# Optimization experiments

Hardware: AMD Instinct MI355X
Metric: run time of the kernel (lower is better)

The kernel has to match this reference:

```python
import jax, jax.numpy as jnp
import numpy as np
from jax import lax

L1_DECAY = 1e-06


def _maxpool2(x):
    # NCHW 2x2 max pool, stride 2
    return lax.reduce_window(x, -jnp.inf, lax.max, (1, 1, 2, 2), (1, 1, 2, 2), 'VALID')


def _cnn(x, w1, b1, w2, b2, wo, bo):
    # x: [N,128,128] -> [N,64], z-score normalized over batch dim
    x = x[:, None]  # [N,1,128,128]
    dn = ('NCHW', 'OIHW', 'NCHW')
    x = lax.conv_general_dilated(x, w1, (1, 1), 'SAME', dimension_numbers=dn) + b1[None, :, None, None]
    x = _maxpool2(jax.nn.relu(x))  # [N,4,64,64]
    x = lax.conv_general_dilated(x, w2, (1, 1), 'SAME', dimension_numbers=dn) + b2[None, :, None, None]
    x = _maxpool2(jax.nn.relu(x))  # [N,8,32,32]
    x = x.reshape(x.shape[0], -1)  # [N,8192] (C,H,W order, as torch .view)
    x = x @ wo.T + bo  # [N,64]
    mean = x.mean(axis=0)
    std = x.std(axis=0, ddof=1)  # torch unbiased std
    return (x - mean) / std


def _interact(item, nbr):
    # item: [N,64]; nbr: [N,H,K,64]. dot-attention over K per node/hop.
    scores = jnp.einsum('nhkd,nd->nhk', nbr, item)
    attn = jax.nn.softmax(scores, axis=-1)
    return jnp.einsum('nhk,nhkd->nhd', attn, nbr)  # [N,H,64]


def setup_inputs() -> dict:
    key = jax.random.key(0)
    ks = jax.random.split(key, 16)
    B = 4096
    inp = {}
    inp['data'] = jax.random.randint(ks[0], (B, 3), 0, 76)
    inp['cell_nbr'] = jax.random.randint(ks[1], (76, 2, 128), 0, 15970)
    inp['drug_nbr'] = jax.random.randint(ks[2], (764, 2, 128), 0, 15970)
    inp['protein_table'] = jax.random.normal(ks[3], (15970, 64), jnp.float32)
    inp['cell_emb_pre'] = jax.random.normal(ks[4], (76, 128, 128), jnp.float32)
    inp['drug_emb_pre'] = jax.random.normal(ks[5], (764, 128, 128), jnp.float32)
    inp['conv1_w'] = 0.05 * jax.random.normal(ks[6], (4, 1, 3, 3), jnp.float32)
    inp['conv1_b'] = 0.05 * jax.random.normal(ks[7], (4,), jnp.float32)
    inp['conv2_w'] = 0.05 * jax.random.normal(ks[8], (8, 4, 3, 3), jnp.float32)
    inp['conv2_b'] = 0.05 * jax.random.normal(ks[9], (8,), jnp.float32)
    inp['out_w'] = 0.05 * jax.random.normal(ks[10], (64, 8192), jnp.float32)
    inp['out_b'] = 0.05 * jax.random.normal(ks[11], (64,), jnp.float32)
    inp['agg_w'] = 0.05 * jax.random.normal(ks[12], (64, 128), jnp.float32)
    inp['agg_b'] = 0.05 * jax.random.normal(ks[13], (64,), jnp.float32)
    inp['comb_w'] = 0.05 * jax.random.normal(ks[14], (64, 128), jnp.float32)
    return inp


def reference(data, cell_nbr, drug_nbr, protein_table, cell_emb_pre, drug_emb_pre,
              conv1_w, conv1_b, conv2_w, conv2_b, out_w, out_b, agg_w, agg_b, comb_w):
    cells, drug1, drug2 = data[:, 0], data[:, 1], data[:, 2]
    B = data.shape[0]

    # per-node neighbor embedding gather: [num, n_hop, K, 64]
    cell_nbr_emb = protein_table[cell_nbr]
    drug_nbr_emb = protein_table[drug_nbr]

    # CNN item embeddings from precomputed images
    cell_item = _cnn(cell_emb_pre, conv1_w, conv1_b, conv2_w, conv2_b, out_w, out_b)  # [76,64]
    drug_item = _cnn(drug_emb_pre, conv1_w, conv1_b, conv2_w, conv2_b, out_w, out_b)  # [764,64]

    # gather -> attend -> weighted sum, then concat hops and aggregate
    cell_i = _interact(cell_item, cell_nbr_emb).reshape(cell_item.shape[0], -1)  # [76,128]
    drug_i = _interact(drug_item, drug_nbr_emb).reshape(drug_item.shape[0], -1)  # [764,128]
    cell_emb = cell_i @ agg_w.T + agg_b  # [76,64]
    drug_emb = drug_i @ agg_w.T + agg_b  # [764,64]

    # batch gather, keep singleton dim 1 to match torch stacking of [1,64]
    ce = cell_emb[cells][:, None, :]   # [B,1,64]
    d1e = drug_emb[drug1][:, None, :]
    d2e = drug_emb[drug2][:, None, :]

    # therapy: transformation_matrix
    combined = jnp.concatenate([d1e, d2e], axis=2) @ comb_w.T  # [B,1,64]
    therapy = (combined * ce).sum(axis=2)  # [B,1]
    toxic = (d1e * d2e).sum(axis=2)        # [B,1]
    score = therapy - toxic

    # emb loss (faithful to source: neighbor lists are indexed on the BATCH dim by hop)
    cnl = cell_nbr_emb[cells]   # [B,2,128,64]
    dnl1 = drug_nbr_emb[drug1]
    dnl2 = drug_nbr_emb[drug2]
    sq = lambda t: jnp.sum(t * t)
    item_reg = (sq(ce) + sq(d1e) + sq(d2e)) / 2
    node_reg = jnp.float32(0.0)
    for hop in range(2):
        node_reg = node_reg + (sq(cnl[hop]) + sq(dnl1[hop]) + sq(dnl2[hop])) / 2
    emb_loss = L1_DECAY * (item_reg + node_reg) / B
    return score, emb_loss
```

## Files before the change

### kernel.cpp

```cpp
#include <hip/hip_runtime.h>
#include <hip/hip_bf16.h>
#include <math.h>

#define N_CELL 76
#define N_DRUG 764
#define N_ITEM 840
#define BATCH  4096

#define POOL2H_B 55050240u
#define POOL2L_B 68812800u
#define WHI_B    0u
#define WLO_B    1048576u
#define XFC_B    2097152u
#define ITEM_B   2312192u
#define EMB_B    2527232u
#define V_B      2742272u
#define LOSS_B   2781184u

typedef short bh8 __attribute__((ext_vector_type(8)));
typedef short bh4 __attribute__((ext_vector_type(4)));
typedef float f32x4 __attribute__((ext_vector_type(4)));

static __device__ inline unsigned short f2bf(float f) {
  union { float f; unsigned u; } v; v.f = f;
  unsigned r = v.u + 0x7FFFu + ((v.u >> 16) & 1u);
  return (unsigned short)(r >> 16);
}
static __device__ inline float bf2f(unsigned short h) {
  union { unsigned u; float f; } v; v.u = ((unsigned)h) << 16;
  return v.f;
}
static __device__ inline unsigned short f2bf_lo(float f, unsigned short h) {
  union { float f; unsigned u; } a; a.f = f - bf2f(h);
  return (unsigned short)(a.u >> 16);
}

union BH8U { bh8 v; struct { bh4 lo, hi; } s; };

__global__ __launch_bounds__(256) void k_conv1(
    const float* __restrict__ cell_pre, const float* __restrict__ drug_pre,
    const float* __restrict__ w1, const float* __restrict__ b1,
    float* __restrict__ pool1) {
  __shared__ unsigned short lh[34 * 34 * 4];
  __shared__ unsigned short ll[34 * 34 * 4];
  int quarter = blockIdx.x, n = blockIdx.y;
  int tid = threadIdx.x;
  int cy0 = quarter * 32;
  const float4* src = (const float4*)((n < N_CELL) ? (cell_pre + (size_t)n * 16384)
                                                   : (drug_pre + (size_t)(n - N_CELL) * 16384));
  for (int i = tid; i < 34 * 32; i += 256) {
    int lr = i >> 5, g = i & 31;
    int iy = cy0 - 1 + lr;
    float4 v = make_float4(0.f, 0.f, 0.f, 0.f);
    if (iy >= 0 && iy < 128) v = src[iy * 32 + g];
    ushort4 h, l;
    h.x = f2bf(v.x); l.x = f2bf_lo(v.x, h.x);
    h.y = f2bf(v.y); l.y = f2bf_lo(v.y, h.y);
    h.z = f2bf(v.z); l.z = f2bf_lo(v.z, h.z);
    h.w = f2bf(v.w); l.w = f2bf_lo(v.w, h.w);
    ((ushort4*)lh)[lr * 34 + g + 1] = h;
    ((ushort4*)ll)[lr * 34 + g + 1] = l;
  }
  if (tid < 68) {
    int lr = tid >> 1, g = (tid & 1) ? 33 : 0;
    ushort4 z = make_ushort4(0, 0, 0, 0);
    ((ushort4*)lh)[lr * 34 + g] = z;
    ((ushort4*)ll)[lr * 34 + g] = z;
  }
  int wv_ = tid >> 6;
  int lane = tid & 63;
  int ml = lane & 15, q = lane >> 4;
  int oc = ml & 3, yv = (ml >> 2) & 1, hi = ml >> 3;
  float bb = b1[oc];
  bh8 BhE, BlE, BhO, BlO;
  {
    int kr = q - yv;
    bool krok = (kr >= 0 && kr <= 2);
#pragma unroll
    for (int j = 0; j < 8; ++j) {
      float ve = 0.f, vo = 0.f;
      if (krok) {
        int kse = j - 3 - 2 * hi;
        int kso = j - 2 * hi;
        if (kse >= 0 && kse <= 2) ve = w1[oc * 9 + kr * 3 + kse];
        if (kso >= 0 && kso <= 2) vo = w1[oc * 9 + kr * 3 + kso];
      }
      unsigned short he = f2bf(ve), ho = f2bf(vo);
      BhE[j] = (short)he; BlE[j] = (short)f2bf_lo(ve, he);
      BhO[j] = (short)ho; BlO[j] = (short)f2bf_lo(vo, ho);
    }
  }
  __syncthreads();
  int x0 = (wv_ & 1) * 16;
  int rp0 = (wv_ >> 1) * 8;
  int Lb = x0 + ml;
  const bh4* lh4 = (const bh4*)lh;
  const bh4* ll4 = (const bh4*)ll;
#pragma unroll 1
  for (int i = 0; i < 8; ++i) {
    int rp = rp0 + i;
    int lr = 2 * rp + q;
    int base = lr * 34 + Lb;
    bh4 g0h = lh4[base], g1h = lh4[base + 1], g2h = lh4[base + 2];
    bh4 g0l = ll4[base], g1l = ll4[base + 1], g2l = ll4[base + 2];
    BH8U aeh, ael, aoh, aol;
    aeh.s.lo = g0h; aeh.s.hi = g1h;
    ael.s.lo = g0l; ael.s.hi = g1l;
    aoh.s.lo = g1h; aoh.s.hi = g2h;
    aol.s.lo = g1l; aol.s.hi = g2l;
    f32x4 de = {0.f, 0.f, 0.f, 0.f}, dd = de;
    de = __builtin_amdgcn_mfma_f32_16x16x32_bf16(aeh.v, BhE, de, 0, 0, 0);
    de = __builtin_amdgcn_mfma_f32_16x16x32_bf16(aeh.v, BlE, de, 0, 0, 0);
    de = __builtin_amdgcn_mfma_f32_16x16x32_bf16(ael.v, BhE, de, 0, 0, 0);
    dd = __builtin_amdgcn_mfma_f32_16x16x32_bf16(aoh.v, BhO, dd, 0, 0, 0);
    dd = __builtin_amdgcn_mfma_f32_16x16x32_bf16(aoh.v, BlO, dd, 0, 0, 0);
    dd = __builtin_amdgcn_mfma_f32_16x16x32_bf16(aol.v, BhO, dd, 0, 0, 0);
    int py = quarter * 16 + rp;
#pragma unroll
    for (int r = 0; r < 4; ++r) {
      float t = fmaxf(de[r], dd[r]);
      float t2 = __shfl_xor(t, 4);
      if (yv == 0) {
        float val = fmaxf(fmaxf(t, t2) + bb, 0.f);
        int px = 2 * (x0 + q * 4 + r) + hi;
        pool1[(((size_t)n * 64 + py) * 64 + px) * 4 + oc] = val;
      }
    }
  }
}

__global__ __launch_bounds__(256) void k_conv2(
    const float* __restrict__ pool1, const float* __restrict__ w2,
    const float* __restrict__ b2, unsigned short* __restrict__ pool2h,
    unsigned short* __restrict__ pool2l) {
  __shared__ unsigned short lh[18 * 66 * 4];
  __shared__ unsigned short ll[18 * 66 * 4];
  int quarter = blockIdx.x, n = blockIdx.y;
  int tid = threadIdx.x;
  int cy0 = quarter * 16;
  const float4* src = (const float4*)(pool1 + (size_t)n * 16384);
  for (int i = tid; i < 18 * 64; i += 256) {
    int r = i >> 6, c = i & 63;
    int iy = cy0 - 1 + r;
    float4 v = make_float4(0.f, 0.f, 0.f, 0.f);
    if (iy >= 0 && iy < 64) v = src[iy * 64 + c];
    ushort4 h, l;
    h.x = f2bf(v.x); l.x = f2bf_lo(v.x, h.x);
    h.y = f2bf(v.y); l.y = f2bf_lo(v.y, h.y);
    h.z = f2bf(v.z); l.z = f2bf_lo(v.z, h.z);
    h.w = f2bf(v.w); l.w = f2bf_lo(v.w, h.w);
    ((ushort4*)lh)[r * 66 + c + 1] = h;
    ((ushort4*)ll)[r * 66 + c + 1] = l;
  }
  if (tid < 36) {
    int r = tid >> 1, c = (tid & 1) ? 65 : 0;
    ushort4 z = make_ushort4(0, 0, 0, 0);
    ((ushort4*)lh)[r * 66 + c] = z;
    ((ushort4*)ll)[r * 66 + c] = z;
  }
  int wv_ = tid >> 6;
  int lane = tid & 63;
  int ml = lane & 15, q = lane >> 4;
  int oc_b = ml & 7, yv = ml >> 3;
  bh8 Bh[2], Bl[2];
#pragma unroll
  for (int ch = 0; ch < 2; ++ch) {
#pragma unroll
    for (int j = 0; j < 8; ++j) {
      int kg = ch * 32 + q * 8 + j;
      float v = 0.f;
      if (kg < 48) {
        int r = kg / 12, rem = kg - r * 12;
        int ks = rem >> 2, ic = rem & 3;
        int kr = r - yv;
        if (kr >= 0 && kr <= 2) v = w2[(oc_b * 4 + ic) * 9 + kr * 3 + ks];
      } else if (kg == 48) {
        v = b2[oc_b];
      }
      unsigned short h = f2bf(v);
      Bh[ch][j] = (short)h;
      Bl[ch][j] = (short)f2bf_lo(v, h);
    }
  }
  int c0 = 2 * q, c1 = 2 * q + 1;
  int c2 = 8 + 2 * q, c3 = 9 + 2 * q;
  if (c2 > 11) { c2 = 8; c3 = 9; }
  int r0 = (c0 * 86) >> 8, s0 = c0 - 3 * r0;
  int r1 = (c1 * 86) >> 8, s1 = c1 - 3 * r1;
  int r2 = (c2 * 86) >> 8, s2 = c2 - 3 * r2;
  int r3 = (c3 * 86) >> 8, s3 = c3 - 3 * r3;
  int x0 = (wv_ & 3) << 4;
  int off0 = r0 * 66 + x0 + ml + s0;
  int off1 = r1 * 66 + x0 + ml + s1;
  int off2 = r2 * 66 + x0 + ml + s2;
  int off3 = r3 * 66 + x0 + ml + s3;
  __syncthreads();
  const bh4* lh4 = (const bh4*)lh;
  const bh4* ll4 = (const bh4*)ll;
#pragma unroll 1
  for (int rp = 0; rp < 8; ++rp) {
    int base = 2 * rp * 66;
    BH8U ah0, al0, ah1, al1;
    ah0.s.lo = lh4[base + off0]; ah0.s.hi = lh4[base + off1];
    al0.s.lo = ll4[base + off0]; al0.s.hi = ll4[base + off1];
    if (q < 2) {
      ah1.s.lo = lh4[base + off2]; ah1.s.hi = lh4[base + off3];
      al1.s.lo = ll4[base + off2]; al1.s.hi = ll4[base + off3];
    } else {
#pragma unroll
      for (int j = 0; j < 8; ++j) { ah1.v[j] = 0; al1.v[j] = 0; }
      if (q == 2) ah1.v[0] = (short)0x3F80;
    }
    f32x4 accA = {0.f, 0.f, 0.f, 0.f}, accB = accA;
    accA = __builtin_amdgcn_mfma_f32_16x16x32_bf16(ah0.v, Bh[0], accA, 0, 0, 0);
    accA = __builtin_amdgcn_mfma_f32_16x16x32_bf16(ah0.v, Bl[0], accA, 0, 0, 0);
    accA = __builtin_amdgcn_mfma_f32_16x16x32_bf16(al0.v, Bh[0], accA, 0, 0, 0);
    accB = __builtin_amdgcn_mfma_f32_16x16x32_bf16(ah1.v, Bh[1], accB, 0, 0, 0);
    accB = __builtin_amdgcn_mfma_f32_16x16x32_bf16(ah1.v, Bl[1], accB, 0, 0, 0);
    accB = __builtin_amdgcn_mfma_f32_16x16x32_bf16(al1.v, Bh[1], accB, 0, 0, 0);
    float d0 = accA[0] + accB[0], d1 = accA[1] + accB[1];
    float d2 = accA[2] + accB[2], d3 = accA[3] + accB[3];
    float m0 = fmaxf(d0, d1), m1 = fmaxf(d2, d3);
    float o0 = __shfl_xor(m0, 8), o1 = __shfl_xor(m1, 8);
    m0 = fmaxf(fmaxf(m0, o0), 0.f);
    m1 = fmaxf(fmaxf(m1, o1), 0.f);
    if (yv == 0) {
      unsigned short h0 = f2bf(m0), h1 = f2bf(m1);
      unsigned short l0 = f2bf(m0 - bf2f(h0)), l1 = f2bf(m1 - bf2f(h1));
      int PR = quarter * 8 + rp;
      unsigned ui = (unsigned)n * 4096u + (unsigned)oc_b * 512u +
                    (unsigned)PR * 16u + (unsigned)(x0 >> 2) + (unsigned)q;
      ((unsigned*)pool2h)[ui] = (unsigned)h0 | ((unsigned)h1 << 16);
      ((unsigned*)pool2l)[ui] = (unsigned)l0 | ((unsigned)l1 << 16);
    }
  }
}

__global__ __launch_bounds__(256) void k_cast(
    const float* __restrict__ out_w, unsigned short* __restrict__ whi,
    unsigned short* __restrict__ wlo, float* __restrict__ xfc,
    float* __restrict__ loss) {
  int gid = blockIdx.x * 256 + threadIdx.x;
  if (gid == 0) *loss = 0.f;
  float4 v = ((const float4*)out_w)[gid];
  ushort4 h, l;
  h.x = f2bf(v.x); l.x = f2bf(v.x - bf2f(h.x));
  h.y = f2bf(v.y); l.y = f2bf(v.y - bf2f(h.y));
  h.z = f2bf(v.z); l.z = f2bf(v.z - bf2f(h.z));
  h.w = f2bf(v.w); l.w = f2bf(v.w - bf2f(h.w));
  ((ushort4*)whi)[gid] = h;
  ((ushort4*)wlo)[gid] = l;
  if (gid < N_ITEM * 64) xfc[gid] = 0.f;
}

__global__ __launch_bounds__(64) void k_fc(
    const unsigned short* __restrict__ pool2h, const unsigned short* __restrict__ pool2l,
    const unsigned short* __restrict__ whi, const unsigned short* __restrict__ wlo,
    float* __restrict__ xfc) {
  int mt = blockIdx.x, kc = blockIdx.y;
  int lane = threadIdx.x;
  int ml = lane & 15, q = lane >> 4;
  int row = mt * 16 + ml; if (row > N_ITEM - 1) row = N_ITEM - 1;
  size_t k0 = (size_t)kc * 256 + q * 8;
  const bh8* Ah = (const bh8*)(pool2h + (size_t)row * 8192 + k0);
  const bh8* Al = (const bh8*)(pool2l + (size_t)row * 8192 + k0);
  const bh8* Bh[4], * Bl[4];
#pragma unroll
  for (int nb = 0; nb < 4; ++nb) {
    Bh[nb] = (const bh8*)(whi + (size_t)(nb * 16 + ml) * 8192 + k0);
    Bl[nb] = (const bh8*)(wlo + (size_t)(nb * 16 + ml) * 8192 + k0);
  }
  f32x4 acc[4];
#pragma unroll
  for (int nb = 0; nb < 4; ++nb) acc[nb] = (f32x4){0.f, 0.f, 0.f, 0.f};
#pragma unroll
  for (int st = 0; st < 8; ++st) {
    bh8 ah = Ah[st * 4], al = Al[st * 4];
#pragma unroll
    for (int nb = 0; nb < 4; ++nb) {
      bh8 bhv = Bh[nb][st * 4], blv = Bl[nb][st * 4];
      acc[nb] = __builtin_amdgcn_mfma_f32_16x16x32_bf16(ah, bhv, acc[nb], 0, 0, 0);
      acc[nb] = __builtin_amdgcn_mfma_f32_16x16x32_bf16(ah, blv, acc[nb], 0, 0, 0);
      acc[nb] = __builtin_amdgcn_mfma_f32_16x16x32_bf16(al, bhv, acc[nb], 0, 0, 0);
    }
  }
#pragma unroll
  for (int r = 0; r < 4; ++r) {
    int mr = mt * 16 + q * 4 + r;
    if (mr < N_ITEM) {
      float* dst = xfc + (size_t)mr * 64 + ml;
#pragma unroll
      for (int nb = 0; nb < 4; ++nb) atomicAdd(dst + nb * 16, acc[nb][r]);
    }
  }
}

__global__ __launch_bounds__(256) void k_norm(
    const float* __restrict__ xfc, float* __restrict__ item) {
  __shared__ float red[256];
  int grp = blockIdx.x >> 6;
  int o = blockIdx.x & 63;
  int base = grp ? N_CELL : 0;
  int N = grp ? N_DRUG : N_CELL;
  int tid = threadIdx.x;
  float s = 0.f;
  for (int i = tid; i < N; i += 256) s += xfc[(size_t)(base + i) * 64 + o];
  red[tid] = s; __syncthreads();
  for (int w = 128; w > 0; w >>= 1) { if (tid < w) red[tid] += red[tid + w]; __syncthreads(); }
  float mean = red[0] / (float)N;
  __syncthreads();
  float sq = 0.f;
  for (int i = tid; i < N; i += 256) {
    float d = xfc[(size_t)(base + i) * 64 + o] - mean;
    sq += d * d;
  }
  red[tid] = sq; __syncthreads();
  for (int w = 128; w > 0; w >>= 1) { if (tid < w) red[tid] += red[tid + w]; __syncthreads(); }
  float inv_std = 1.f / sqrtf(red[0] / (float)(N - 1));
  for (int i = tid; i < N; i += 256)
    item[(size_t)(base + i) * 64 + o] = (xfc[(size_t)(base + i) * 64 + o] - mean) * inv_std;
}

__global__ __launch_bounds__(256) void k_interact(
    const int* __restrict__ cell_nbr, const int* __restrict__ drug_nbr,
    const float* __restrict__ protein, const float* __restrict__ item,
    const float* __restrict__ agg_w, const float* __restrict__ agg_b,
    float* __restrict__ emb) {
  __shared__ float pb[128 * 65];
  __shared__ float item_s[64];
  __shared__ float sc[128];
  __shared__ float hop_out[128];
  __shared__ float red[256];
  int n = blockIdx.x;
  int tid = threadIdx.x;
  const int* nbr = (n < N_CELL) ? (cell_nbr + (size_t)n * 256)
                                : (drug_nbr + (size_t)(n - N_CELL) * 256);
  if (tid < 64) item_s[tid] = item[(size_t)n * 64 + tid];
  __syncthreads();
  for (int h = 0; h < 2; ++h) {
    for (int e = tid; e < 8192; e += 256) {
      int k = e >> 6, d = e & 63;
      int idx = nbr[h * 128 + k];
      pb[k * 65 + d] = protein[(size_t)idx * 64 + d];
    }
    __syncthreads();
    {
      int k = tid >> 1, halfd = tid & 1;
      int d0 = halfd * 32;
      float p = 0.f;
#pragma unroll
      for (int d = 0; d < 32; ++d) p += item_s[d0 + d] * pb[k * 65 + d0 + d];
      p += __shfl_xor(p, 1);
      if (halfd == 0) sc[k] = p;
    }
    __syncthreads();
    if (tid < 64) {
      float a = sc[tid], b = sc[tid + 64];
      float m = fmaxf(a, b);
#pragma unroll
      for (int off = 32; off > 0; off >>= 1) m = fmaxf(m, __shfl_xor(m, off));
      float e0 = __expf(a - m), e1 = __expf(b - m);
      float s = e0 + e1;
#pragma unroll
      for (int off = 32; off > 0; off >>= 1) s += __shfl_xor(s, off);
      float inv = 1.f / s;
      sc[tid] = e0 * inv; sc[tid + 64] = e1 * inv;
    }
    __syncthreads();
    {
      int d = tid & 63, kq = tid >> 6;
      float p = 0.f;
#pragma unroll
      for (int k = 0; k < 32; ++k) {
        int kk = kq * 32 + k;
        p += sc[kk] * pb[kk * 65 + d];
      }
      red[tid] = p;
    }
    __syncthreads();
    if (tid < 64)
      hop_out[h * 64 + tid] = red[tid] + red[tid + 64] + red[tid + 128] + red[tid + 192];
    __syncthreads();
  }
  {
    int o = tid & 63, jq = tid >> 6;
    float p = 0.f;
#pragma unroll
    for (int j = 0; j < 32; ++j) {
      int jj = jq * 32 + j;
      p += hop_out[jj] * agg_w[(size_t)o * 128 + jj];
    }
    red[tid] = p;
  }
  __syncthreads();
  if (tid < 64)
    emb[(size_t)n * 64 + tid] =
        red[tid] + red[tid + 64] + red[tid + 128] + red[tid + 192] + agg_b[tid];
}

__global__ __launch_bounds__(128) void k_cellv(
    const float* __restrict__ emb, const float* __restrict__ comb_w,
    float* __restrict__ V) {
  __shared__ float ce[64];
  int c = blockIdx.x;
  int j = threadIdx.x;
  if (j < 64) ce[j] = emb[(size_t)c * 64 + j];
  __syncthreads();
  float s = 0.f;
#pragma unroll
  for (int o = 0; o < 64; ++o) s += comb_w[(size_t)o * 128 + j] * ce[o];
  V[(size_t)c * 128 + j] = s;
}

__global__ __launch_bounds__(256) void k_score(
    const int* __restrict__ data, const float* __restrict__ emb,
    const float* __restrict__ V, float* __restrict__ out,
    float* __restrict__ loss) {
  __shared__ float racc[4];
  int tid = threadIdx.x;
  int lane = tid & 63;
  int w = tid >> 6;
  int b = blockIdx.x * 4 + w;
  int c = data[b * 3 + 0], d1 = data[b * 3 + 1], d2 = data[b * 3 + 2];
  float ce = emb[(size_t)c * 64 + lane];
  float e1 = emb[(size_t)(N_CELL + d1) * 64 + lane];
  float e2 = emb[(size_t)(N_CELL + d2) * 64 + lane];
  float v1 = V[(size_t)c * 128 + lane];
  float v2 = V[(size_t)c * 128 + 64 + lane];
  float th = e1 * v1 + e2 * v2;
  float tx = e1 * e2;
  float rg = ce * ce + e1 * e1 + e2 * e2;
#pragma unroll
  for (int off = 32; off > 0; off >>= 1) {
    th += __shfl_xor(th, off);
    tx += __shfl_xor(tx, off);
    rg += __shfl_xor(rg, off);
  }
  if (lane == 0) { out[b] = th - tx; racc[w] = rg; }
  __syncthreads();
  if (tid == 0) atomicAdd(loss, 0.5f * (racc[0] + racc[1] + racc[2] + racc[3]));
}

__global__ __launch_bounds__(256) void k_nodereg(
    const int* __restrict__ data, const int* __restrict__ cell_nbr,
    const int* __restrict__ drug_nbr, const float* __restrict__ protein,
    float* __restrict__ loss) {
  __shared__ float red[256];
  int j = blockIdx.x;
  int hop = j / 3, which = j % 3;
  int row = data[hop * 3 + which];
  const int* nbr = (which == 0) ? (cell_nbr + (size_t)row * 256)
                                : (drug_nbr + (size_t)row * 256);
  int tid = threadIdx.x;
  float acc = 0.f;
  for (int e = tid; e < 16384; e += 256) {
    int k = e >> 6, d = e & 63;
    float v = protein[(size_t)nbr[k] * 64 + d];
    acc += v * v;
  }
  red[tid] = acc; __syncthreads();
  for (int w = 128; w > 0; w >>= 1) { if (tid < w) red[tid] += red[tid + w]; __syncthreads(); }
  if (tid == 0) atomicAdd(loss, 0.5f * red[0]);
}

__global__ void k_finalize(const float* __restrict__ loss, float* __restrict__ out) {
  if (threadIdx.x == 0) out[BATCH] = loss[0] * (1e-6f / 4096.f);
}

extern "C" void kernel_launch(void* const* d_in, const int* in_sizes, int n_in,
                              void* d_out, int out_size, void* d_ws, size_t ws_size,
                              hipStream_t stream) {
  const int*   data      = (const int*)d_in[0];
  const int*   cell_nbr  = (const int*)d_in[1];
  const int*   drug_nbr  = (const int*)d_in[2];
  const float* protein   = (const float*)d_in[3];
  const float* cell_pre  = (const float*)d_in[4];
  const float* drug_pre  = (const float*)d_in[5];
  const float* w1        = (const float*)d_in[6];
  const float* b1        = (const float*)d_in[7];
  const float* w2        = (const float*)d_in[8];
  const float* b2        = (const float*)d_in[9];
  const float* out_w     = (const float*)d_in[10];
  const float* agg_w     = (const float*)d_in[12];
  const float* agg_b     = (const float*)d_in[13];
  const float* comb_w    = (const float*)d_in[14];
  float* out = (float*)d_out;
  char* base = (char*)d_ws;
  float* pool1            = (float*)base;
  unsigned short* pool2h  = (unsigned short*)(base + POOL2H_B);
  unsigned short* pool2l  = (unsigned short*)(base + POOL2L_B);
  unsigned short* whi     = (unsigned short*)(base + WHI_B);
  unsigned short* wlo     = (unsigned short*)(base + WLO_B);
  float* xfc              = (float*)(base + XFC_B);
  float* item             = (float*)(base + ITEM_B);
  float* emb              = (float*)(base + EMB_B);
  float* V                = (float*)(base + V_B);
  float* loss             = (float*)(base + LOSS_B);

  k_conv1<<<dim3(4, 840), 256, 0, stream>>>(cell_pre, drug_pre, w1, b1, pool1);
  k_conv2<<<dim3(4, 840), 256, 0, stream>>>(pool1, w2, b2, pool2h, pool2l);
  k_cast<<<512, 256, 0, stream>>>(out_w, whi, wlo, xfc, loss);
  k_fc<<<dim3(53, 32), 64, 0, stream>>>(pool2h, pool2l, whi, wlo, xfc);
  k_norm<<<128, 256, 0, stream>>>(xfc, item);
  k_interact<<<840, 256, 0, stream>>>(cell_nbr, drug_nbr, protein, item, agg_w, agg_b, emb);
  k_cellv<<<N_CELL, 128, 0, stream>>>(emb, comb_w, V);
  k_score<<<1024, 256, 0, stream>>>(data, emb, V, out, loss);
  k_nodereg<<<6, 256, 0, stream>>>(data, cell_nbr, drug_nbr, protein, loss);
  k_finalize<<<1, 64, 0, stream>>>(loss, out);
}
```

Before: 250.3 us.

## Fuse conv1 into conv2 via shared-memory halo and merge small tail kernels

Conv1 and conv2 become one kernel. Each block computes conv1 over a halo of pooled rows and keeps the pooled result in LDS as split bf16, so the 55MB fp32 pool1 intermediate is no longer written and re-read through global memory. The weight cast and xfc zeroing run in extra blocks of the same grid. k_cellv is folded into k_interact, and score, node-reg and finalize are merged into one kernel that uses an atomic counter for the last-block finalize. In exchange, conv1 does some redundant halo compute, LDS use per block goes up (which may lower occupancy), and the kernel count drops from 10 to 5.

```diff
diff --git a/kernel.cpp b/kernel.cpp
--- a/kernel.cpp
+++ b/kernel.cpp
@@ -7,15 +7,16 @@
 #define N_ITEM 840
 #define BATCH  4096
 
-#define POOL2H_B 55050240u
-#define POOL2L_B 68812800u
-#define WHI_B    0u
-#define WLO_B    1048576u
-#define XFC_B    2097152u
-#define ITEM_B   2312192u
-#define EMB_B    2527232u
-#define V_B      2742272u
-#define LOSS_B   2781184u
+#define POOL2H_B 0u
+#define POOL2L_B 13762560u
+#define WHI_B    27525120u
+#define WLO_B    28573696u
+#define XFC_B    29622272u
+#define ITEM_B   29837312u
+#define EMB_B    30052352u
+#define V_B      30267392u
+#define LOSS_B   30306304u
+#define CNT_B    30306368u
 
 typedef short bh8 __attribute__((ext_vector_type(8)));
 typedef short bh4 __attribute__((ext_vector_type(4)));
@@ -37,20 +38,44 @@
 
 union BH8U { bh8 v; struct { bh4 lo, hi; } s; };
 
-__global__ __launch_bounds__(256) void k_conv1(
+__global__ __launch_bounds__(256) void k_conv12(
     const float* __restrict__ cell_pre, const float* __restrict__ drug_pre,
     const float* __restrict__ w1, const float* __restrict__ b1,
-    float* __restrict__ pool1) {
-  __shared__ unsigned short lh[34 * 34 * 4];
-  __shared__ unsigned short ll[34 * 34 * 4];
-  int quarter = blockIdx.x, n = blockIdx.y;
+    const float* __restrict__ w2, const float* __restrict__ b2,
+    const float* __restrict__ out_w,
+    unsigned short* __restrict__ pool2h, unsigned short* __restrict__ pool2l,
+    unsigned short* __restrict__ whi, unsigned short* __restrict__ wlo,
+    float* __restrict__ xfc, float* __restrict__ loss, unsigned* __restrict__ cnt) {
+  __shared__ unsigned short slh[38 * 34 * 4];
+  __shared__ unsigned short sll[38 * 34 * 4];
+  __shared__ unsigned short p1h[18 * 66 * 4];
+  __shared__ unsigned short p1l[18 * 66 * 4];
+  int n = blockIdx.y;
   int tid = threadIdx.x;
-  int cy0 = quarter * 32;
+  if (n >= 840) {
+    int cb = (n - 840) * 4 + blockIdx.x;
+    int gid = cb * 256 + tid;
+    if (gid == 0) { *loss = 0.f; *cnt = 0u; }
+    for (int i = gid; i < 13440; i += 5120)
+      ((float4*)xfc)[i] = make_float4(0.f, 0.f, 0.f, 0.f);
+    for (int i = gid; i < 131072; i += 5120) {
+      float4 v = ((const float4*)out_w)[i];
+      ushort4 h, l;
+      h.x = f2bf(v.x); l.x = f2bf(v.x - bf2f(h.x));
+      h.y = f2bf(v.y); l.y = f2bf(v.y - bf2f(h.y));
+      h.z = f2bf(v.z); l.z = f2bf(v.z - bf2f(h.z));
+      h.w = f2bf(v.w); l.w = f2bf(v.w - bf2f(h.w));
+      ((ushort4*)whi)[i] = h;
+      ((ushort4*)wlo)[i] = l;
+    }
+    return;
+  }
+  int qt = blockIdx.x;
   const float4* src = (const float4*)((n < N_CELL) ? (cell_pre + (size_t)n * 16384)
                                                    : (drug_pre + (size_t)(n - N_CELL) * 16384));
-  for (int i = tid; i < 34 * 32; i += 256) {
+  for (int i = tid; i < 38 * 32; i += 256) {
     int lr = i >> 5, g = i & 31;
-    int iy = cy0 - 1 + lr;
+    int iy = qt * 32 - 3 + lr;
     float4 v = make_float4(0.f, 0.f, 0.f, 0.f);
     if (iy >= 0 && iy < 128) v = src[iy * 32 + g];
     ushort4 h, l;
@@ -58,23 +83,30 @@
     h.y = f2bf(v.y); l.y = f2bf_lo(v.y, h.y);
     h.z = f2bf(v.z); l.z = f2bf_lo(v.z, h.z);
     h.w = f2bf(v.w); l.w = f2bf_lo(v.w, h.w);
-    ((ushort4*)lh)[lr * 34 + g + 1] = h;
-    ((ushort4*)ll)[lr * 34 + g + 1] = l;
-  }
-  if (tid < 68) {
+    ((ushort4*)slh)[lr * 34 + g + 1] = h;
+    ((ushort4*)sll)[lr * 34 + g + 1] = l;
+  }
+  if (tid < 76) {
     int lr = tid >> 1, g = (tid & 1) ? 33 : 0;
     ushort4 z = make_ushort4(0, 0, 0, 0);
-    ((ushort4*)lh)[lr * 34 + g] = z;
-    ((ushort4*)ll)[lr * 34 + g] = z;
-  }
-  int wv_ = tid >> 6;
+    ((ushort4*)slh)[lr * 34 + g] = z;
+    ((ushort4*)sll)[lr * 34 + g] = z;
+  }
+  if (tid < 36) {
+    int r = tid >> 1, c = (tid & 1) ? 65 : 0;
+    ushort4 z = make_ushort4(0, 0, 0, 0);
+    ((ushort4*)p1h)[r * 66 + c] = z;
+    ((ushort4*)p1l)[r * 66 + c] = z;
+  }
+  int wv = tid >> 6;
   int lane = tid & 63;
   int ml = lane & 15, q = lane >> 4;
-  int oc = ml & 3, yv = (ml >> 2) & 1, hi = ml >> 3;
+
+  int oc = ml & 3, yv1 = (ml >> 2) & 1, hi = ml >> 3;
   float bb = b1[oc];
   bh8 BhE, BlE, BhO, BlO;
   {
-    int kr = q - yv;
+    int kr = q - yv1;
     bool krok = (kr >= 0 && kr <= 2);
 #pragma unroll
     for (int j = 0; j < 8; ++j) {
@@ -90,17 +122,50 @@
       BhO[j] = (short)ho; BlO[j] = (short)f2bf_lo(vo, ho);
     }
   }
+  int oc_b = ml & 7, yv2 = ml >> 3;
+  bh8 Bh2[2], Bl2[2];
+#pragma unroll
+  for (int ch = 0; ch < 2; ++ch) {
+#pragma unroll
+    for (int j = 0; j < 8; ++j) {
+      int kg = ch * 32 + q * 8 + j;
+      float v = 0.f;
+      if (kg < 48) {
+        int r = kg / 12, rem = kg - r * 12;
+        int ks = rem >> 2, ic = rem & 3;
+        int kr = r - yv2;
+        if (kr >= 0 && kr <= 2) v = w2[(oc_b * 4 + ic) * 9 + kr * 3 + ks];
+      } else if (kg == 48) {
+        v = b2[oc_b];
+      }
+      unsigned short h = f2bf(v);
+      Bh2[ch][j] = (short)h;
+      Bl2[ch][j] = (short)f2bf_lo(v, h);
+    }
+  }
+  int c0 = 2 * q, c1 = 2 * q + 1;
+  int c2 = 8 + 2 * q, c3 = 9 + 2 * q;
+  if (c2 > 11) { c2 = 8; c3 = 9; }
+  int r0 = (c0 * 86) >> 8, s0 = c0 - 3 * r0;
+  int r1 = (c1 * 86) >> 8, s1 = c1 - 3 * r1;
+  int r2 = (c2 * 86) >> 8, s2 = c2 - 3 * r2;
+  int r3 = (c3 * 86) >> 8, s3 = c3 - 3 * r3;
+  int x2 = (wv & 3) << 4;
+  int off0 = r0 * 66 + x2 + ml + s0;
+  int off1 = r1 * 66 + x2 + ml + s1;
+  int off2 = r2 * 66 + x2 + ml + s2;
+  int off3 = r3 * 66 + x2 + ml + s3;
   __syncthreads();
-  int x0 = (wv_ & 1) * 16;
-  int rp0 = (wv_ >> 1) * 8;
+
+  int x0 = (wv & 1) * 16;
+  int rbase = (wv >> 1) * 9;
   int Lb = x0 + ml;
-  const bh4* lh4 = (const bh4*)lh;
-  const bh4* ll4 = (const bh4*)ll;
+  const bh4* lh4 = (const bh4*)slh;
+  const bh4* ll4 = (const bh4*)sll;
 #pragma unroll 1
-  for (int i = 0; i < 8; ++i) {
-    int rp = rp0 + i;
-    int lr = 2 * rp + q;
-    int base = lr * 34 + Lb;
+  for (int ii = 0; ii < 9; ++ii) {
+    int i = rbase + ii;
+    int base = (2 * i + q) * 34 + Lb;
     bh4 g0h = lh4[base], g1h = lh4[base + 1], g2h = lh4[base + 2];
     bh4 g0l = ll4[base], g1l = ll4[base + 1], g2l = ll4[base + 2];
     BH8U aeh, ael, aoh, aol;
@@ -115,142 +180,64 @@
     dd = __builtin_amdgcn_mfma_f32_16x16x32_bf16(aoh.v, BhO, dd, 0, 0, 0);
     dd = __builtin_amdgcn_mfma_f32_16x16x32_bf16(aoh.v, BlO, dd, 0, 0, 0);
     dd = __builtin_amdgcn_mfma_f32_16x16x32_bf16(aol.v, BhO, dd, 0, 0, 0);
-    int py = quarter * 16 + rp;
+    int pr = qt * 16 - 1 + i;
+    bool inr = (pr >= 0 && pr < 64);
 #pragma unroll
     for (int r = 0; r < 4; ++r) {
       float t = fmaxf(de[r], dd[r]);
       float t2 = __shfl_xor(t, 4);
-      if (yv == 0) {
+      if (yv1 == 0) {
         float val = fmaxf(fmaxf(t, t2) + bb, 0.f);
+        if (!inr) val = 0.f;
+        unsigned short h = f2bf(val);
+        unsigned short l = f2bf_lo(val, h);
         int px = 2 * (x0 + q * 4 + r) + hi;
-        pool1[(((size_t)n * 64 + py) * 64 + px) * 4 + oc] = val;
+        int idx = (i * 66 + px + 1) * 4 + oc;
+        p1h[idx] = h; p1l[idx] = l;
       }
     }
   }
-}
-
-__global__ __launch_bounds__(256) void k_conv2(
-    const float* __restrict__ pool1, const float* __restrict__ w2,
-    const float* __restrict__ b2, unsigned short* __restrict__ pool2h,
-    unsigned short* __restrict__ pool2l) {
-  __shared__ unsigned short lh[18 * 66 * 4];
-  __shared__ unsigned short ll[18 * 66 * 4];
-  int quarter = blockIdx.x, n = blockIdx.y;
-  int tid = threadIdx.x;
-  int cy0 = quarter * 16;
-  const float4* src = (const float4*)(pool1 + (size_t)n * 16384);
-  for (int i = tid; i < 18 * 64; i += 256) {
-    int r = i >> 6, c = i & 63;
-    int iy = cy0 - 1 + r;
-    float4 v = make_float4(0.f, 0.f, 0.f, 0.f);
-    if (iy >= 0 && iy < 64) v = src[iy * 64 + c];
-    ushort4 h, l;
-    h.x = f2bf(v.x); l.x = f2bf_lo(v.x, h.x);
-    h.y = f2bf(v.y); l.y = f2bf_lo(v.y, h.y);
-    h.z = f2bf(v.z); l.z = f2bf_lo(v.z, h.z);
-    h.w = f2bf(v.w); l.w = f2bf_lo(v.w, h.w);
-    ((ushort4*)lh)[r * 66 + c + 1] = h;
-    ((ushort4*)ll)[r * 66 + c + 1] = l;
-  }
-  if (tid < 36) {
-    int r = tid >> 1, c = (tid & 1) ? 65 : 0;
-    ushort4 z = make_ushort4(0, 0, 0, 0);
-    ((ushort4*)lh)[r * 66 + c] = z;
-    ((ushort4*)ll)[r * 66 + c] = z;
-  }
-  int wv_ = tid >> 6;
-  int lane = tid & 63;
-  int ml = lane & 15, q = lane >> 4;
-  int oc_b = ml & 7, yv = ml >> 3;
-  bh8 Bh[2], Bl[2];
-#pragma unroll
-  for (int ch = 0; ch < 2; ++ch) {
-#pragma unroll
-    for (int j = 0; j < 8; ++j) {
-      int kg = ch * 32 + q * 8 + j;
-      float v = 0.f;
-      if (kg < 48) {
-        int r = kg / 12, rem = kg - r * 12;
-        int ks = rem >> 2, ic = rem & 3;
-        int kr = r - yv;
-        if (kr >= 0 && kr <= 2) v = w2[(oc_b * 4 + ic) * 9 + kr * 3 + ks];
-      } else if (kg == 48) {
-        v = b2[oc_b];
-      }
-      unsigned short h = f2bf(v);
-      Bh[ch][j] = (short)h;
-      Bl[ch][j] = (short)f2bf_lo(v, h);
-    }
-  }
-  int c0 = 2 * q, c1 = 2 * q + 1;
-  int c2 = 8 + 2 * q, c3 = 9 + 2 * q;
-  if (c2 > 11) { c2 = 8; c3 = 9; }
-  int r0 = (c0 * 86) >> 8, s0 = c0 - 3 * r0;
-  int r1 = (c1 * 86) >> 8, s1 = c1 - 3 * r1;
-  int r2 = (c2 * 86) >> 8, s2 = c2 - 3 * r2;
-  int r3 = (c3 * 86) >> 8, s3 = c3 - 3 * r3;
-  int x0 = (wv_ & 3) << 4;
-  int off0 = r0 * 66 + x0 + ml + s0;
-  int off1 = r1 * 66 + x0 + ml + s1;
-  int off2 = r2 * 66 + x0 + ml + s2;
-  int off3 = r3 * 66 + x0 + ml + s3;
   __syncthreads();
-  const bh4* lh4 = (const bh4*)lh;
-  const bh4* ll4 = (const bh4*)ll;
+
+  const bh4* ph4 = (const bh4*)p1h;
+  const bh4* pl4 = (const bh4*)p1l;
 #pragma unroll 1
   for (int rp = 0; rp < 8; ++rp) {
-    int base = 2 * rp * 66;
+    int base2 = 2 * rp * 66;
     BH8U ah0, al0, ah1, al1;
-    ah0.s.lo = lh4[base + off0]; ah0.s.hi = lh4[base + off1];
-    al0.s.lo = ll4[base + off0]; al0.s.hi = ll4[base + off1];
+    ah0.s.lo = ph4[base2 + off0]; ah0.s.hi = ph4[base2 + off1];
+    al0.s.lo = pl4[base2 + off0]; al0.s.hi = pl4[base2 + off1];
     if (q < 2) {
-      ah1.s.lo = lh4[base + off2]; ah1.s.hi = lh4[base + off3];
-      al1.s.lo = ll4[base + off2]; al1.s.hi = ll4[base + off3];
+      ah1.s.lo = ph4[base2 + off2]; ah1.s.hi = ph4[base2 + off3];
+      al1.s.lo = pl4[base2 + off2]; al1.s.hi = pl4[base2 + off3];
     } else {
 #pragma unroll
       for (int j = 0; j < 8; ++j) { ah1.v[j] = 0; al1.v[j] = 0; }
       if (q == 2) ah1.v[0] = (short)0x3F80;
     }
     f32x4 accA = {0.f, 0.f, 0.f, 0.f}, accB = accA;
-    accA = __builtin_amdgcn_mfma_f32_16x16x32_bf16(ah0.v, Bh[0], accA, 0, 0, 0);
-    accA = __builtin_amdgcn_mfma_f32_16x16x32_bf16(ah0.v, Bl[0], accA, 0, 0, 0);
-    accA = __builtin_amdgcn_mfma_f32_16x16x32_bf16(al0.v, Bh[0], accA, 0, 0, 0);
-    accB = __builtin_amdgcn_mfma_f32_16x16x32_bf16(ah1.v, Bh[1], accB, 0, 0, 0);
-    accB = __builtin_amdgcn_mfma_f32_16x16x32_bf16(ah1.v, Bl[1], accB, 0, 0, 0);
-    accB = __builtin_amdgcn_mfma_f32_16x16x32_bf16(al1.v, Bh[1], accB, 0, 0, 0);
+    accA = __builtin_amdgcn_mfma_f32_16x16x32_bf16(ah0.v, Bh2[0], accA, 0, 0, 0);
+    accA = __builtin_amdgcn_mfma_f32_16x16x32_bf16(ah0.v, Bl2[0], accA, 0, 0, 0);
+    accA = __builtin_amdgcn_mfma_f32_16x16x32_bf16(al0.v, Bh2[0], accA, 0, 0, 0);
+    accB = __builtin_amdgcn_mfma_f32_16x16x32_bf16(ah1.v, Bh2[1], accB, 0, 0, 0);
+    accB = __builtin_amdgcn_mfma_f32_16x16x32_bf16(ah1.v, Bl2[1], accB, 0, 0, 0);
+    accB = __builtin_amdgcn_mfma_f32_16x16x32_bf16(al1.v, Bh2[1], accB, 0, 0, 0);
     float d0 = accA[0] + accB[0], d1 = accA[1] + accB[1];
     float d2 = accA[2] + accB[2], d3 = accA[3] + accB[3];
     float m0 = fmaxf(d0, d1), m1 = fmaxf(d2, d3);
     float o0 = __shfl_xor(m0, 8), o1 = __shfl_xor(m1, 8);
     m0 = fmaxf(fmaxf(m0, o0), 0.f);
     m1 = fmaxf(fmaxf(m1, o1), 0.f);
-    if (yv == 0) {
+    if (yv2 == 0) {
       unsigned short h0 = f2bf(m0), h1 = f2bf(m1);
       unsigned short l0 = f2bf(m0 - bf2f(h0)), l1 = f2bf(m1 - bf2f(h1));
-      int PR = quarter * 8 + rp;
+      int PR = qt * 8 + rp;
       unsigned ui = (unsigned)n * 4096u + (unsigned)oc_b * 512u +
-                    (unsigned)PR * 16u + (unsigned)(x0 >> 2) + (unsigned)q;
+                    (unsigned)PR * 16u + (unsigned)(x2 >> 2) + (unsigned)q;
       ((unsigned*)pool2h)[ui] = (unsigned)h0 | ((unsigned)h1 << 16);
       ((unsigned*)pool2l)[ui] = (unsigned)l0 | ((unsigned)l1 << 16);
     }
   }
-}
-
-__global__ __launch_bounds__(256) void k_cast(
-    const float* __restrict__ out_w, unsigned short* __restrict__ whi,
-    unsigned short* __restrict__ wlo, float* __restrict__ xfc,
-    float* __restrict__ loss) {
-  int gid = blockIdx.x * 256 + threadIdx.x;
-  if (gid == 0) *loss = 0.f;
-  float4 v = ((const float4*)out_w)[gid];
-  ushort4 h, l;
-  h.x = f2bf(v.x); l.x = f2bf(v.x - bf2f(h.x));
-  h.y = f2bf(v.y); l.y = f2bf(v.y - bf2f(h.y));
-  h.z = f2bf(v.z); l.z = f2bf(v.z - bf2f(h.z));
-  h.w = f2bf(v.w); l.w = f2bf(v.w - bf2f(h.w));
-  ((ushort4*)whi)[gid] = h;
-  ((ushort4*)wlo)[gid] = l;
-  if (gid < N_ITEM * 64) xfc[gid] = 0.f;
 }
 
 __global__ __launch_bounds__(64) void k_fc(
@@ -325,12 +312,14 @@
     const int* __restrict__ cell_nbr, const int* __restrict__ drug_nbr,
     const float* __restrict__ protein, const float* __restrict__ item,
     const float* __restrict__ agg_w, const float* __restrict__ agg_b,
-    float* __restrict__ emb) {
+    const float* __restrict__ comb_w, float* __restrict__ emb,
+    float* __restrict__ V) {
   __shared__ float pb[128 * 65];
   __shared__ float item_s[64];
   __shared__ float sc[128];
   __shared__ float hop_out[128];
   __shared__ float red[256];
+  __shared__ float emb_f[64];
   int n = blockIdx.x;
   int tid = threadIdx.x;
   const int* nbr = (n < N_CELL) ? (cell_nbr + (size_t)n * 256)
@@ -393,78 +382,76 @@
     red[tid] = p;
   }
   __syncthreads();
-  if (tid < 64)
-    emb[(size_t)n * 64 + tid] =
-        red[tid] + red[tid + 64] + red[tid + 128] + red[tid + 192] + agg_b[tid];
-}
-
-__global__ __launch_bounds__(128) void k_cellv(
-    const float* __restrict__ emb, const float* __restrict__ comb_w,
-    float* __restrict__ V) {
-  __shared__ float ce[64];
-  int c = blockIdx.x;
-  int j = threadIdx.x;
-  if (j < 64) ce[j] = emb[(size_t)c * 64 + j];
-  __syncthreads();
-  float s = 0.f;
-#pragma unroll
-  for (int o = 0; o < 64; ++o) s += comb_w[(size_t)o * 128 + j] * ce[o];
-  V[(size_t)c * 128 + j] = s;
-}
-
-__global__ __launch_bounds__(256) void k_score(
-    const int* __restrict__ data, const float* __restrict__ emb,
-    const float* __restrict__ V, float* __restrict__ out,
-    float* __restrict__ loss) {
-  __shared__ float racc[4];
-  int tid = threadIdx.x;
-  int lane = tid & 63;
-  int w = tid >> 6;
-  int b = blockIdx.x * 4 + w;
-  int c = data[b * 3 + 0], d1 = data[b * 3 + 1], d2 = data[b * 3 + 2];
-  float ce = emb[(size_t)c * 64 + lane];
-  float e1 = emb[(size_t)(N_CELL + d1) * 64 + lane];
-  float e2 = emb[(size_t)(N_CELL + d2) * 64 + lane];
-  float v1 = V[(size_t)c * 128 + lane];
-  float v2 = V[(size_t)c * 128 + 64 + lane];
-  float th = e1 * v1 + e2 * v2;
-  float tx = e1 * e2;
-  float rg = ce * ce + e1 * e1 + e2 * e2;
-#pragma unroll
-  for (int off = 32; off > 0; off >>= 1) {
-    th += __shfl_xor(th, off);
-    tx += __shfl_xor(tx, off);
-    rg += __shfl_xor(rg, off);
-  }
-  if (lane == 0) { out[b] = th - tx; racc[w] = rg; }
-  __syncthreads();
-  if (tid == 0) atomicAdd(loss, 0.5f * (racc[0] + racc[1] + racc[2] + racc[3]));
-}
-
-__global__ __launch_bounds__(256) void k_nodereg(
+  if (tid < 64) {
+    float ev = red[tid] + red[tid + 64] + red[tid + 128] + red[tid + 192] + agg_b[tid];
+    emb[(size_t)n * 64 + tid] = ev;
+    emb_f[tid] = ev;
+  }
+  if (n < N_CELL) {
+    __syncthreads();
+    if (tid < 128) {
+      float s = 0.f;
+#pragma unroll
+      for (int o = 0; o < 64; ++o) s += comb_w[(size_t)o * 128 + tid] * emb_f[o];
+      V[(size_t)n * 128 + tid] = s;
+    }
+  }
+}
+
+__global__ __launch_bounds__(256) void k_scoreall(
     const int* __restrict__ data, const int* __restrict__ cell_nbr,
     const int* __restrict__ drug_nbr, const float* __restrict__ protein,
-    float* __restrict__ loss) {
+    const float* __restrict__ emb, const float* __restrict__ V,
+    float* __restrict__ out, float* __restrict__ loss, unsigned* __restrict__ cnt) {
   __shared__ float red[256];
-  int j = blockIdx.x;
-  int hop = j / 3, which = j % 3;
-  int row = data[hop * 3 + which];
-  const int* nbr = (which == 0) ? (cell_nbr + (size_t)row * 256)
-                                : (drug_nbr + (size_t)row * 256);
+  int bx = blockIdx.x;
   int tid = threadIdx.x;
-  float acc = 0.f;
-  for (int e = tid; e < 16384; e += 256) {
-    int k = e >> 6, d = e & 63;
-    float v = protein[(size_t)nbr[k] * 64 + d];
-    acc += v * v;
-  }
-  red[tid] = acc; __syncthreads();
-  for (int w = 128; w > 0; w >>= 1) { if (tid < w) red[tid] += red[tid + w]; __syncthreads(); }
-  if (tid == 0) atomicAdd(loss, 0.5f * red[0]);
-}
-
-__global__ void k_finalize(const float* __restrict__ loss, float* __restrict__ out) {
-  if (threadIdx.x == 0) out[BATCH] = loss[0] * (1e-6f / 4096.f);
+  if (bx < 1024) {
+    int lane = tid & 63;
+    int w = tid >> 6;
+    int b = bx * 4 + w;
+    int c = data[b * 3 + 0], d1 = data[b * 3 + 1], d2 = data[b * 3 + 2];
+    float ce = emb[(size_t)c * 64 + lane];
+    float e1 = emb[(size_t)(N_CELL + d1) * 64 + lane];
+    float e2 = emb[(size_t)(N_CELL + d2) * 64 + lane];
+    float v1 = V[(size_t)c * 128 + lane];
+    float v2 = V[(size_t)c * 128 + 64 + lane];
+    float th = e1 * v1 + e2 * v2;
+    float tx = e1 * e2;
+    float rg = ce * ce + e1 * e1 + e2 * e2;
+#pragma unroll
+    for (int off = 32; off > 0; off >>= 1) {
+      th += __shfl_xor(th, off);
+      tx += __shfl_xor(tx, off);
+      rg += __shfl_xor(rg, off);
+    }
+    if (lane == 0) { out[b] = th - tx; red[w] = rg; }
+    __syncthreads();
+    if (tid == 0) atomicAdd(loss, 0.5f * (red[0] + red[1] + red[2] + red[3]));
+  } else {
+    int j = bx - 1024;
+    int hop = j / 3, which = j % 3;
+    int row = data[hop * 3 + which];
+    const int* nbr = (which == 0) ? (cell_nbr + (size_t)row * 256)
+                                  : (drug_nbr + (size_t)row * 256);
+    float acc = 0.f;
+    for (int e = tid; e < 16384; e += 256) {
+      int k = e >> 6, d = e & 63;
+      float v = protein[(size_t)nbr[k] * 64 + d];
+      acc += v * v;
+    }
+    red[tid] = acc; __syncthreads();
+    for (int w = 128; w > 0; w >>= 1) { if (tid < w) red[tid] += red[tid + w]; __syncthreads(); }
+    if (tid == 0) atomicAdd(loss, 0.5f * red[0]);
+  }
+  if (tid == 0) {
+    __threadfence();
+    unsigned old = atomicAdd(cnt, 1u);
+    if (old == gridDim.x - 1) {
+      float L = atomicAdd(loss, 0.f);
+      out[BATCH] = L * (1e-6f / 4096.f);
+    }
+  }
 }
 
 extern "C" void kernel_launch(void* const* d_in, const int* in_sizes, int n_in,
@@ -486,7 +473,6 @@
   const float* comb_w    = (const float*)d_in[14];
   float* out = (float*)d_out;
   char* base = (char*)d_ws;
-  float* pool1            = (float*)base;
   unsigned short* pool2h  = (unsigned short*)(base + POOL2H_B);
   unsigned short* pool2l  = (unsigned short*)(base + POOL2L_B);
   unsigned short* whi     = (unsigned short*)(base + WHI_B);
@@ -496,15 +482,13 @@
   float* emb              = (float*)(base + EMB_B);
   float* V                = (float*)(base + V_B);
   float* loss             = (float*)(base + LOSS_B);
-
-  k_conv1<<<dim3(4, 840), 256, 0, stream>>>(cell_pre, drug_pre, w1, b1, pool1);
-  k_conv2<<<dim3(4, 840), 256, 0, stream>>>(pool1, w2, b2, pool2h, pool2l);
-  k_cast<<<512, 256, 0, stream>>>(out_w, whi, wlo, xfc, loss);
+  unsigned* cnt           = (unsigned*)(base + CNT_B);
+
+  k_conv12<<<dim3(4, 845), 256, 0, stream>>>(cell_pre, drug_pre, w1, b1, w2, b2, out_w,
+                                             pool2h, pool2l, whi, wlo, xfc, loss, cnt);
   k_fc<<<dim3(53, 32), 64, 0, stream>>>(pool2h, pool2l, whi, wlo, xfc);
   k_norm<<<128, 256, 0, stream>>>(xfc, item);
-  k_interact<<<840, 256, 0, stream>>>(cell_nbr, drug_nbr, protein, item, agg_w, agg_b, emb);
-  k_cellv<<<N_CELL, 128, 0, stream>>>(emb, comb_w, V);
-  k_score<<<1024, 256, 0, stream>>>(data, emb, V, out, loss);
-  k_nodereg<<<6, 256, 0, stream>>>(data, cell_nbr, drug_nbr, protein, loss);
-  k_finalize<<<1, 64, 0, stream>>>(loss, out);
-}
+  k_interact<<<840, 256, 0, stream>>>(cell_nbr, drug_nbr, protein, item, agg_w, agg_b,
+                                      comb_w, emb, V);
+  k_scoreall<<<1030, 256, 0, stream>>>(data, cell_nbr, drug_nbr, protein, emb, V, out, loss, cnt);
+}
```

After: 253.2 us. About the same (+1.2%).
